# Kernel optimization log

Measured on AMD Instinct MI355X. Metric: run time of the kernel, lower is better.

## Reference

```python
import jax, jax.numpy as jnp
import numpy as np

N_NODES = 100000
N_EDGES = 1600000
IN, HID, OUT = 128, 64, 64


def setup_inputs() -> dict:
    key = jax.random.key(0)
    ks = jax.random.split(key, 7)
    features = jax.random.normal(ks[0], (N_NODES, IN), dtype=jnp.float32)
    src = jax.random.randint(ks[1], (N_EDGES,), 0, N_NODES, dtype=jnp.int64)
    dst = jax.random.randint(ks[2], (N_EDGES,), 0, N_NODES, dtype=jnp.int64)
    # glorot-uniform-like init for GraphConv weights
    lim1 = np.sqrt(6.0 / (IN + HID)).astype(np.float32)
    lim2 = np.sqrt(6.0 / (HID + OUT)).astype(np.float32)
    W1 = jax.random.uniform(ks[3], (IN, HID), jnp.float32, -lim1, lim1)
    b1 = jnp.zeros((HID,), jnp.float32)
    W2 = jax.random.uniform(ks[4], (HID, OUT), jnp.float32, -lim2, lim2)
    b2 = jnp.zeros((OUT,), jnp.float32)
    return {"features": features, "src": src, "dst": dst,
            "W1": W1, "b1": b1, "W2": W2, "b2": b2}


def _graph_conv(h, W, b, src, dst, out_norm, in_norm, relu, n_nodes):
    # DGL GraphConv, norm='both':
    #   h_src *= outdeg^{-1/2}; aggregate sum over edges; h_dst *= indeg^{-1/2}
    #   W applied before aggregation if in_feats > out_feats (fewer bytes moved)
    h = h * out_norm[:, None]
    if h.shape[1] > W.shape[1]:
        h = h @ W
        agg = jax.ops.segment_sum(h[src], dst, num_segments=n_nodes)
    else:
        agg = jax.ops.segment_sum(h[src], dst, num_segments=n_nodes)
        agg = agg @ W
    out = agg * in_norm[:, None] + b
    return jax.nn.relu(out) if relu else out


def reference(features, src, dst, W1, b1, W2, b2):
    n_nodes = features.shape[0]
    ones = jnp.ones(src.shape[0], features.dtype)
    out_deg = jnp.maximum(jax.ops.segment_sum(ones, src, num_segments=n_nodes), 1.0)
    in_deg = jnp.maximum(jax.ops.segment_sum(ones, dst, num_segments=n_nodes), 1.0)
    out_norm = jax.lax.rsqrt(out_deg)
    in_norm = jax.lax.rsqrt(in_deg)
    h = _graph_conv(features, W1, b1, src, dst, out_norm, in_norm, True, n_nodes)
    # Dropout(0.5) between layers: identity in eval mode
    h = _graph_conv(h, W2, b2, src, dst, out_norm, in_norm, False, n_nodes)
    return h
```

## Files before the change

kernel.cpp:

```cpp
#include <hip/hip_runtime.h>
#include <hip/hip_fp16.h>

#define NCH 64
#define INF 128
#define PAD 64
#define HQD 128
#define HQS 64
#define NPH 2
#define CHUNK_H 50000
#define NPF 8
#define CHUNK_F 12500

using ivec4 = __attribute__((ext_vector_type(4))) int;
using hvec8 = __attribute__((ext_vector_type(8))) _Float16;
using fvec8 = __attribute__((ext_vector_type(8))) float;
using half8 = __attribute__((ext_vector_type(8))) _Float16;
using f32x4 = __attribute__((ext_vector_type(4))) float;

__global__ __launch_bounds__(512) void k_hist2(
    const int* __restrict__ src, const int* __restrict__ dst,
    unsigned char* __restrict__ shist, unsigned char* __restrict__ dhist,
    int nE, int nN) {
    __shared__ unsigned cnt[CHUNK_H / 4];
    const int dstBlocks = NPH * HQD;
    const bool isDst = (int)blockIdx.x < dstBlocks;
    const int bid = isDst ? blockIdx.x : blockIdx.x - dstBlocks;
    const int* __restrict__ arr = isDst ? dst : src;
    unsigned char* __restrict__ hist = isDst ? dhist : shist;
    const int HQX = isDst ? HQD : HQS;
    const int p = bid & (NPH - 1);
    const int q = bid >> 1;
    const int lo = p * CHUNK_H;
    for (int i = threadIdx.x; i < CHUNK_H / 4; i += 512) cnt[i] = 0;
    __syncthreads();
    const int nE4 = nE >> 2;
    const int b0 = (int)(((long)q * nE4) / HQX);
    const int b1 = (int)(((long)(q + 1) * nE4) / HQX);
    for (int i = b0 + threadIdx.x; i < b1; i += 512) {
        ivec4 v4 = __builtin_nontemporal_load(((const ivec4*)arr) + i);
#pragma unroll
        for (int j = 0; j < 4; ++j) {
            int x = v4[j] - lo;
            if ((unsigned)x < (unsigned)CHUNK_H)
                atomicAdd(&cnt[x >> 2], 1u << ((x & 3) * 8));
        }
    }
    if (q == 0 && threadIdx.x < (nE & 3)) {
        int x = arr[(nE4 << 2) + threadIdx.x] - lo;
        if ((unsigned)x < (unsigned)CHUNK_H)
            atomicAdd(&cnt[x >> 2], 1u << ((x & 3) * 8));
    }
    __syncthreads();
    unsigned* hp = (unsigned*)(hist + (long)q * nN + lo);
    int lim = nN - lo;
    if (lim > CHUNK_H) lim = CHUNK_H;
    lim >>= 2;
    for (int i = threadIdx.x; i < lim; i += 512) hp[i] = cnt[i];
}

__global__ void k_scan2(const unsigned char* __restrict__ shist,
                        unsigned char* __restrict__ dhist,
                        float* __restrict__ onorm, int* __restrict__ indeg, int nN) {
    int n = blockIdx.x * blockDim.x + threadIdx.x;
    if (n >= nN) return;
    int s = 0;
#pragma unroll 4
    for (int q = 0; q < HQS; ++q) s += shist[(long)q * nN + n];
    onorm[n] = rsqrtf(fmaxf((float)s, 1.0f));
    int run = 0;
    for (int q = 0; q < HQD; ++q) {
        long idx = (long)q * nN + n;
        int v = dhist[idx];
        dhist[idx] = (unsigned char)run;
        run += v;
    }
    indeg[n] = run;
}

__global__ __launch_bounds__(512) void k_fill(
    const int* __restrict__ src, const int* __restrict__ dst,
    const unsigned char* __restrict__ qoff, int* __restrict__ ell, int nE, int nN) {
    __shared__ unsigned cnt[CHUNK_F / 4];
    const int p = blockIdx.x & (NPF - 1);
    const int q = blockIdx.x >> 3;
    const int lo = p * CHUNK_F;
    const unsigned* qw = (const unsigned*)(qoff + (long)q * nN + lo);
    for (int i = threadIdx.x; i < CHUNK_F / 4; i += 512) cnt[i] = qw[i];
    __syncthreads();
    const int nE4 = nE >> 2;
    const int b0 = (int)(((long)q * nE4) / HQD);
    const int b1 = (int)(((long)(q + 1) * nE4) / HQD);
    for (int i = b0 + threadIdx.x; i < b1; i += 512) {
        ivec4 s4 = __builtin_nontemporal_load(((const ivec4*)src) + i);
        ivec4 d4 = __builtin_nontemporal_load(((const ivec4*)dst) + i);
#pragma unroll
        for (int j = 0; j < 4; ++j) {
            int d = d4[j] - lo;
            if ((unsigned)d < (unsigned)CHUNK_F) {
                int sh = (d & 3) * 8;
                unsigned old = atomicAdd(&cnt[d >> 2], 1u << sh);
                int pos = (old >> sh) & 0xff;
                if (pos < PAD) ell[(long)(lo + d) * PAD + pos] = s4[j];
            }
        }
    }
    if (q == 0 && threadIdx.x < (nE & 3)) {
        int e = (nE4 << 2) + threadIdx.x;
        int d = dst[e] - lo;
        if ((unsigned)d < (unsigned)CHUNK_F) {
            int sh = (d & 3) * 8;
            unsigned old = atomicAdd(&cnt[d >> 2], 1u << sh);
            int pos = (old >> sh) & 0xff;
            if (pos < PAD) ell[(long)(lo + d) * PAD + pos] = src[e];
        }
    }
}

__global__ __launch_bounds__(256) void k_gemm1m(
    const float* __restrict__ feat, const float* __restrict__ W1,
    const float* __restrict__ onorm, __half* __restrict__ h1, int nN)
{
    const int lane = threadIdx.x & 63;
    const int row_in = lane & 15;
    const int kgrp = lane >> 4;
    half8 bf[4][4];
#pragma unroll
    for (int ks = 0; ks < 4; ++ks)
#pragma unroll
        for (int g = 0; g < 4; ++g) {
            int col = g * 16 + row_in;
#pragma unroll
            for (int j = 0; j < 8; ++j)
                bf[ks][g][j] = (_Float16)W1[(ks * 32 + kgrp * 8 + j) * NCH + col];
        }
    const int nTiles = (nN + 15) >> 4;
    int tile = blockIdx.x * 4 + (threadIdx.x >> 6);
    const int stride = gridDim.x * 4;
    for (; tile < nTiles; tile += stride) {
        const long r0 = (long)tile * 16;
        const long ra = r0 + row_in;
        half8 af[4];
        if (ra < nN) {
#pragma unroll
            for (int ks = 0; ks < 4; ++ks) {
                const float* fp = feat + ra * INF + ks * 32 + kgrp * 8;
                float4 x = *(const float4*)fp;
                float4 y = *(const float4*)(fp + 4);
                af[ks][0] = (_Float16)x.x; af[ks][1] = (_Float16)x.y;
                af[ks][2] = (_Float16)x.z; af[ks][3] = (_Float16)x.w;
                af[ks][4] = (_Float16)y.x; af[ks][5] = (_Float16)y.y;
                af[ks][6] = (_Float16)y.z; af[ks][7] = (_Float16)y.w;
            }
        } else {
#pragma unroll
            for (int ks = 0; ks < 4; ++ks)
#pragma unroll
                for (int j = 0; j < 8; ++j) af[ks][j] = (_Float16)0.0f;
        }
        f32x4 acc[4] = {{0,0,0,0},{0,0,0,0},{0,0,0,0},{0,0,0,0}};
#pragma unroll
        for (int ks = 0; ks < 4; ++ks)
#pragma unroll
            for (int g = 0; g < 4; ++g)
                acc[g] = __builtin_amdgcn_mfma_f32_16x16x32_f16(af[ks], bf[ks][g], acc[g], 0, 0, 0);
#pragma unroll
        for (int j = 0; j < 4; ++j) {
            long r = r0 + kgrp * 4 + j;
            if (r < nN) {
                float on = onorm[r];
#pragma unroll
                for (int g = 0; g < 4; ++g)
                    h1[r * NCH + g * 16 + row_in] = __float2half(acc[g][j] * on);
            }
        }
    }
}

__global__ __launch_bounds__(256) void k_agg1(
    const __half* __restrict__ h1s, const int* __restrict__ indeg,
    const int* __restrict__ ell, const float* __restrict__ onorm,
    const float* __restrict__ b1, __half* __restrict__ h2, int nN)
{
    const int c = threadIdx.x & 7;
    int node = (blockIdx.x << 5) + (threadIdx.x >> 3);
    if (node >= nN) return;
    int n0 = indeg[node];
    int n = (n0 > PAD) ? PAD : n0;
    const int* cols = ell + (long)node * PAD;
    fvec8 acc = {0, 0, 0, 0, 0, 0, 0, 0};
    int i = 0;
    for (; i + 4 <= n; i += 4) {
        int s0 = cols[i], s1 = cols[i + 1], s2 = cols[i + 2], s3 = cols[i + 3];
        hvec8 v0 = ((const hvec8*)h1s)[(long)s0 * 8 + c];
        hvec8 v1 = ((const hvec8*)h1s)[(long)s1 * 8 + c];
        hvec8 v2 = ((const hvec8*)h1s)[(long)s2 * 8 + c];
        hvec8 v3 = ((const hvec8*)h1s)[(long)s3 * 8 + c];
#pragma unroll
        for (int j = 0; j < 8; ++j)
            acc[j] += (float)v0[j] + (float)v1[j] + (float)v2[j] + (float)v3[j];
    }
    for (; i < n; ++i) {
        hvec8 v = ((const hvec8*)h1s)[(long)cols[i] * 8 + c];
#pragma unroll
        for (int j = 0; j < 8; ++j) acc[j] += (float)v[j];
    }
    float inn = rsqrtf(fmaxf((float)n0, 1.0f));
    float onn = onorm[node];
    float4 ba = ((const float4*)b1)[2 * c];
    float4 bb = ((const float4*)b1)[2 * c + 1];
    float bv[8] = {ba.x, ba.y, ba.z, ba.w, bb.x, bb.y, bb.z, bb.w};
    hvec8 st;
#pragma unroll
    for (int j = 0; j < 8; ++j)
        st[j] = (_Float16)(fmaxf(acc[j] * inn + bv[j], 0.0f) * onn);
    ((hvec8*)h2)[(long)node * 8 + c] = st;
}

__global__ __launch_bounds__(256) void k_agg2(
    const __half* __restrict__ h2, const int* __restrict__ indeg,
    const int* __restrict__ ell, __half* __restrict__ agg, int nN)
{
    const int c = threadIdx.x & 7;
    int node = (blockIdx.x << 5) + (threadIdx.x >> 3);
    if (node >= nN) return;
    int n0 = indeg[node];
    int n = (n0 > PAD) ? PAD : n0;
    const int* cols = ell + (long)node * PAD;
    fvec8 acc = {0, 0, 0, 0, 0, 0, 0, 0};
    int i = 0;
    for (; i + 4 <= n; i += 4) {
        int s0 = cols[i], s1 = cols[i + 1], s2 = cols[i + 2], s3 = cols[i + 3];
        hvec8 v0 = ((const hvec8*)h2)[(long)s0 * 8 + c];
        hvec8 v1 = ((const hvec8*)h2)[(long)s1 * 8 + c];
        hvec8 v2 = ((const hvec8*)h2)[(long)s2 * 8 + c];
        hvec8 v3 = ((const hvec8*)h2)[(long)s3 * 8 + c];
#pragma unroll
        for (int j = 0; j < 8; ++j)
            acc[j] += (float)v0[j] + (float)v1[j] + (float)v2[j] + (float)v3[j];
    }
    for (; i < n; ++i) {
        hvec8 v = ((const hvec8*)h2)[(long)cols[i] * 8 + c];
#pragma unroll
        for (int j = 0; j < 8; ++j) acc[j] += (float)v[j];
    }
    hvec8 st;
#pragma unroll
    for (int j = 0; j < 8; ++j) st[j] = (_Float16)acc[j];
    ((hvec8*)agg)[(long)node * 8 + c] = st;
}

__global__ __launch_bounds__(256) void k_gemm2m(
    const __half* __restrict__ agg, const float* __restrict__ W2,
    const int* __restrict__ indeg, const float* __restrict__ b2,
    float* __restrict__ out, int nN)
{
    const int lane = threadIdx.x & 63;
    const int row_in = lane & 15;
    const int kgrp = lane >> 4;
    half8 bf[2][4];
#pragma unroll
    for (int ks = 0; ks < 2; ++ks)
#pragma unroll
        for (int g = 0; g < 4; ++g) {
            int col = g * 16 + row_in;
#pragma unroll
            for (int j = 0; j < 8; ++j)
                bf[ks][g][j] = (_Float16)W2[(ks * 32 + kgrp * 8 + j) * NCH + col];
        }
    float bcol[4];
#pragma unroll
    for (int g = 0; g < 4; ++g) bcol[g] = b2[g * 16 + row_in];
    const int nTiles = (nN + 15) >> 4;
    int tile = blockIdx.x * 4 + (threadIdx.x >> 6);
    const int stride = gridDim.x * 4;
    for (; tile < nTiles; tile += stride) {
        const long r0 = (long)tile * 16;
        const long ra = r0 + row_in;
        half8 af[2];
        if (ra < nN) {
#pragma unroll
            for (int ks = 0; ks < 2; ++ks)
                af[ks] = ((const half8*)agg)[ra * 8 + ks * 4 + kgrp];
        } else {
#pragma unroll
            for (int ks = 0; ks < 2; ++ks)
#pragma unroll
                for (int j = 0; j < 8; ++j) af[ks][j] = (_Float16)0.0f;
        }
        f32x4 acc[4] = {{0,0,0,0},{0,0,0,0},{0,0,0,0},{0,0,0,0}};
#pragma unroll
        for (int ks = 0; ks < 2; ++ks)
#pragma unroll
            for (int g = 0; g < 4; ++g)
                acc[g] = __builtin_amdgcn_mfma_f32_16x16x32_f16(af[ks], bf[ks][g], acc[g], 0, 0, 0);
#pragma unroll
        for (int j = 0; j < 4; ++j) {
            long r = r0 + kgrp * 4 + j;
            if (r < nN) {
                float inn = rsqrtf(fmaxf((float)indeg[r], 1.0f));
#pragma unroll
                for (int g = 0; g < 4; ++g)
                    out[r * NCH + g * 16 + row_in] = acc[g][j] * inn + bcol[g];
            }
        }
    }
}

extern "C" void kernel_launch(void* const* d_in, const int* in_sizes, int n_in,
                              void* d_out, int out_size, void* d_ws, size_t ws_size,
                              hipStream_t stream) {
    const float* feat = (const float*)d_in[0];
    const int* src    = (const int*)d_in[1];
    const int* dst    = (const int*)d_in[2];
    const float* W1   = (const float*)d_in[3];
    const float* b1   = (const float*)d_in[4];
    const float* W2   = (const float*)d_in[5];
    const float* b2   = (const float*)d_in[6];
    float* out        = (float*)d_out;

    const int nN = in_sizes[0] / INF;
    const int nE = in_sizes[1];

    char* p = (char*)d_ws;
    float* onorm  = (float*)p;   p += (size_t)nN * 4;
    int* indeg    = (int*)p;     p += (size_t)nN * 4;
    char* unionp  = p;           p += (size_t)nN * NCH * 2 * 2;
    int* ell      = (int*)p;     p += (size_t)nN * PAD * 4;
    unsigned char* shist = (unsigned char*)unionp;
    unsigned char* dhist = (unsigned char*)unionp + (size_t)HQS * nN;
    __half* h2    = (__half*)unionp;
    __half* agg2  = (__half*)(unionp + (size_t)nN * NCH * 2);
    __half* h1    = (__half*)d_out;

    k_hist2<<<NPH * HQD + NPH * HQS, 512, 0, stream>>>(src, dst, shist, dhist, nE, nN);

    k_scan2<<<(nN + 255) / 256, 256, 0, stream>>>(shist, dhist, onorm, indeg, nN);

    k_gemm1m<<<512, 256, 0, stream>>>(feat, W1, onorm, h1, nN);

    k_fill<<<NPF * HQD, 512, 0, stream>>>(src, dst, dhist, ell, nE, nN);

    k_agg1<<<(nN + 31) / 32, 256, 0, stream>>>(h1, indeg, ell, onorm, b1, h2, nN);

    k_agg2<<<(nN + 31) / 32, 256, 0, stream>>>(h2, indeg, ell, agg2, nN);

    k_gemm2m<<<512, 256, 0, stream>>>(agg2, W2, indeg, b2, out, nN);
}
```

Measured before the change: 168.0 us.

## Fuse layer-2 aggregation with W2 MFMA GEMM via shared memory; halve fill partitions

The second-layer neighbor aggregation and the W2 matrix multiply now run in one kernel. Each block aggregates 64 nodes into a shared-memory fp16 tile, then applies W2 with MFMA and writes the final output. This removes the intermediate agg2 buffer round trip through global memory and one kernel launch. The catch is that every block reloads and converts W2 into registers, and blocks are larger per node group. Separately, the fill kernel uses 4 partitions of 25000 nodes instead of 8, doubling its shared counter array and halving its block count.

```diff
diff --git a/kernel.cpp b/kernel.cpp
--- a/kernel.cpp
+++ b/kernel.cpp
@@ -8,8 +8,8 @@
 #define HQS 64
 #define NPH 2
 #define CHUNK_H 50000
-#define NPF 8
-#define CHUNK_F 12500
+#define NPF 4
+#define CHUNK_F 25000
 
 using ivec4 = __attribute__((ext_vector_type(4))) int;
 using hvec8 = __attribute__((ext_vector_type(8))) _Float16;
@@ -82,7 +82,7 @@
     const unsigned char* __restrict__ qoff, int* __restrict__ ell, int nE, int nN) {
     __shared__ unsigned cnt[CHUNK_F / 4];
     const int p = blockIdx.x & (NPF - 1);
-    const int q = blockIdx.x >> 3;
+    const int q = blockIdx.x >> 2;
     const int lo = p * CHUNK_F;
     const unsigned* qw = (const unsigned*)(qoff + (long)q * nN + lo);
     for (int i = threadIdx.x; i < CHUNK_F / 4; i += 512) cnt[i] = qw[i];
@@ -216,45 +216,47 @@
     ((hvec8*)h2)[(long)node * 8 + c] = st;
 }
 
-__global__ __launch_bounds__(256) void k_agg2(
+__global__ __launch_bounds__(256) void k_agg2g2m(
     const __half* __restrict__ h2, const int* __restrict__ indeg,
-    const int* __restrict__ ell, __half* __restrict__ agg, int nN)
+    const int* __restrict__ ell, const float* __restrict__ W2,
+    const float* __restrict__ b2, float* __restrict__ out, int nN)
 {
+    __shared__ _Float16 sA[64][72];
     const int c = threadIdx.x & 7;
-    int node = (blockIdx.x << 5) + (threadIdx.x >> 3);
-    if (node >= nN) return;
-    int n0 = indeg[node];
-    int n = (n0 > PAD) ? PAD : n0;
-    const int* cols = ell + (long)node * PAD;
-    fvec8 acc = {0, 0, 0, 0, 0, 0, 0, 0};
-    int i = 0;
-    for (; i + 4 <= n; i += 4) {
-        int s0 = cols[i], s1 = cols[i + 1], s2 = cols[i + 2], s3 = cols[i + 3];
-        hvec8 v0 = ((const hvec8*)h2)[(long)s0 * 8 + c];
-        hvec8 v1 = ((const hvec8*)h2)[(long)s1 * 8 + c];
-        hvec8 v2 = ((const hvec8*)h2)[(long)s2 * 8 + c];
-        hvec8 v3 = ((const hvec8*)h2)[(long)s3 * 8 + c];
-#pragma unroll
-        for (int j = 0; j < 8; ++j)
-            acc[j] += (float)v0[j] + (float)v1[j] + (float)v2[j] + (float)v3[j];
-    }
-    for (; i < n; ++i) {
-        hvec8 v = ((const hvec8*)h2)[(long)cols[i] * 8 + c];
-#pragma unroll
-        for (int j = 0; j < 8; ++j) acc[j] += (float)v[j];
-    }
-    hvec8 st;
-#pragma unroll
-    for (int j = 0; j < 8; ++j) st[j] = (_Float16)acc[j];
-    ((hvec8*)agg)[(long)node * 8 + c] = st;
-}
-
-__global__ __launch_bounds__(256) void k_gemm2m(
-    const __half* __restrict__ agg, const float* __restrict__ W2,
-    const int* __restrict__ indeg, const float* __restrict__ b2,
-    float* __restrict__ out, int nN)
-{
+    const int grp = threadIdx.x >> 3;
+    const long base = (long)blockIdx.x * 64;
+#pragma unroll
+    for (int r = 0; r < 2; ++r) {
+        int nl = grp + r * 32;
+        long node = base + nl;
+        fvec8 acc = {0, 0, 0, 0, 0, 0, 0, 0};
+        if (node < nN) {
+            int n0 = indeg[node];
+            int n = (n0 > PAD) ? PAD : n0;
+            const int* cols = ell + node * PAD;
+            int i = 0;
+            for (; i + 4 <= n; i += 4) {
+                int s0 = cols[i], s1 = cols[i + 1], s2 = cols[i + 2], s3 = cols[i + 3];
+                hvec8 v0 = ((const hvec8*)h2)[(long)s0 * 8 + c];
+                hvec8 v1 = ((const hvec8*)h2)[(long)s1 * 8 + c];
+                hvec8 v2 = ((const hvec8*)h2)[(long)s2 * 8 + c];
+                hvec8 v3 = ((const hvec8*)h2)[(long)s3 * 8 + c];
+#pragma unroll
+                for (int j = 0; j < 8; ++j)
+                    acc[j] += (float)v0[j] + (float)v1[j] + (float)v2[j] + (float)v3[j];
+            }
+            for (; i < n; ++i) {
+                hvec8 v = ((const hvec8*)h2)[(long)cols[i] * 8 + c];
+#pragma unroll
+                for (int j = 0; j < 8; ++j) acc[j] += (float)v[j];
+            }
+        }
+#pragma unroll
+        for (int j = 0; j < 8; ++j) sA[nl][c * 8 + j] = (_Float16)acc[j];
+    }
+    __syncthreads();
     const int lane = threadIdx.x & 63;
+    const int wave = threadIdx.x >> 6;
     const int row_in = lane & 15;
     const int kgrp = lane >> 4;
     half8 bf[2][4];
@@ -267,41 +269,24 @@
             for (int j = 0; j < 8; ++j)
                 bf[ks][g][j] = (_Float16)W2[(ks * 32 + kgrp * 8 + j) * NCH + col];
         }
-    float bcol[4];
-#pragma unroll
-    for (int g = 0; g < 4; ++g) bcol[g] = b2[g * 16 + row_in];
-    const int nTiles = (nN + 15) >> 4;
-    int tile = blockIdx.x * 4 + (threadIdx.x >> 6);
-    const int stride = gridDim.x * 4;
-    for (; tile < nTiles; tile += stride) {
-        const long r0 = (long)tile * 16;
-        const long ra = r0 + row_in;
-        half8 af[2];
-        if (ra < nN) {
-#pragma unroll
-            for (int ks = 0; ks < 2; ++ks)
-                af[ks] = ((const half8*)agg)[ra * 8 + ks * 4 + kgrp];
-        } else {
-#pragma unroll
-            for (int ks = 0; ks < 2; ++ks)
-#pragma unroll
-                for (int j = 0; j < 8; ++j) af[ks][j] = (_Float16)0.0f;
-        }
-        f32x4 acc[4] = {{0,0,0,0},{0,0,0,0},{0,0,0,0},{0,0,0,0}};
-#pragma unroll
-        for (int ks = 0; ks < 2; ++ks)
+    half8 af[2];
+#pragma unroll
+    for (int ks = 0; ks < 2; ++ks)
+        af[ks] = *(const half8*)&sA[wave * 16 + row_in][ks * 32 + kgrp * 8];
+    f32x4 acc[4] = {{0,0,0,0},{0,0,0,0},{0,0,0,0},{0,0,0,0}};
+#pragma unroll
+    for (int ks = 0; ks < 2; ++ks)
+#pragma unroll
+        for (int g = 0; g < 4; ++g)
+            acc[g] = __builtin_amdgcn_mfma_f32_16x16x32_f16(af[ks], bf[ks][g], acc[g], 0, 0, 0);
+#pragma unroll
+    for (int j = 0; j < 4; ++j) {
+        long r = base + wave * 16 + kgrp * 4 + j;
+        if (r < nN) {
+            float inn = rsqrtf(fmaxf((float)indeg[r], 1.0f));
 #pragma unroll
             for (int g = 0; g < 4; ++g)
-                acc[g] = __builtin_amdgcn_mfma_f32_16x16x32_f16(af[ks], bf[ks][g], acc[g], 0, 0, 0);
-#pragma unroll
-        for (int j = 0; j < 4; ++j) {
-            long r = r0 + kgrp * 4 + j;
-            if (r < nN) {
-                float inn = rsqrtf(fmaxf((float)indeg[r], 1.0f));
-#pragma unroll
-                for (int g = 0; g < 4; ++g)
-                    out[r * NCH + g * 16 + row_in] = acc[g][j] * inn + bcol[g];
-            }
+                out[r * NCH + g * 16 + row_in] = acc[g][j] * inn + b2[g * 16 + row_in];
         }
     }
 }
@@ -329,7 +314,6 @@
     unsigned char* shist = (unsigned char*)unionp;
     unsigned char* dhist = (unsigned char*)unionp + (size_t)HQS * nN;
     __half* h2    = (__half*)unionp;
-    __half* agg2  = (__half*)(unionp + (size_t)nN * NCH * 2);
     __half* h1    = (__half*)d_out;
 
     k_hist2<<<NPH * HQD + NPH * HQS, 512, 0, stream>>>(src, dst, shist, dhist, nE, nN);
@@ -342,7 +326,5 @@
 
     k_agg1<<<(nN + 31) / 32, 256, 0, stream>>>(h1, indeg, ell, onorm, b1, h2, nN);
 
-    k_agg2<<<(nN + 31) / 32, 256, 0, stream>>>(h2, indeg, ell, agg2, nN);
-
-    k_gemm2m<<<512, 256, 0, stream>>>(agg2, W2, indeg, b2, out, nN);
-}
+    k_agg2g2m<<<(nN + 63) / 64, 256, 0, stream>>>(h2, indeg, ell, W2, b2, out, nN);
+}
```

Result: no change. 168.2 us (+0.1%).
